# Performance work log

Hardware: AMD Instinct MI355X
Metric: run time of the kernel (lower is better)

The kernel has to match this reference:

```python
import jax, jax.numpy as jnp
import numpy as np

PAD0, PAD1 = 2, 1  # Blur pad=(2,1), replicate_pad=False -> upfirdn2d pad
UPSAMPLE_FACTOR = 2


def _make_kernel():
    k = jnp.array([1.0, 3.0, 3.0, 1.0], dtype=jnp.float32)
    k2 = k[None, :] * k[:, None]
    k2 = k2 / jnp.sum(k2)
    return k2 * (UPSAMPLE_FACTOR ** 2)  # (4,4)


def setup_inputs() -> dict:
    key = jax.random.key(0)
    x = jax.random.normal(key, (8, 256, 256, 256), dtype=jnp.float32)
    kernel = _make_kernel()
    return {"x": x, "kernel": kernel}


def reference(x, kernel):
    # upfirdn2d with up=1, down=1, pad=(PAD0, PAD1): zero-pad then true
    # convolution with the FIR kernel (flip == cross-correlation kernel).
    N, C, H, W = x.shape
    kh, kw = kernel.shape
    xp = jnp.pad(x, ((0, 0), (0, 0), (PAD0, PAD1), (PAD0, PAD1)))
    k = jnp.flip(kernel)[None, None, :, :]  # (1,1,kh,kw), true convolution
    # depthwise: fold channels into batch, single-channel conv
    xr = xp.reshape(N * C, 1, H + PAD0 + PAD1, W + PAD0 + PAD1)
    out = jax.lax.conv_general_dilated(
        xr, k, window_strides=(1, 1), padding='VALID',
        dimension_numbers=('NCHW', 'OIHW', 'NCHW'))
    Ho = H + PAD0 + PAD1 - kh + 1
    Wo = W + PAD0 + PAD1 - kw + 1
    return out.reshape(N, C, Ho, Wo)
```

## Files before the change

kernel.cpp:

```cpp
#include <hip/hip_runtime.h>


constexpr int W = 256;
constexpr int H = 256;
constexpr float F0 = 0.25f;
constexpr float F1 = 0.75f;

typedef float f32x4 __attribute__((ext_vector_type(4)));

__device__ __forceinline__ float4 hrow(const float* __restrict__ xp, int i,
                                       int lane, int col) {
    if ((unsigned)i >= (unsigned)H) return make_float4(0.f, 0.f, 0.f, 0.f);
    const float* r = xp + i * W;
    float4 v = *reinterpret_cast<const float4*>(r + col);
    float2 L = *reinterpret_cast<const float2*>(r + (lane ? col - 2 : 0));
    float  R = r[lane < 63 ? col + 4 : W - 1];
    if (lane == 0)  { L.x = 0.f; L.y = 0.f; }
    if (lane == 63) { R = 0.f; }
    float4 h;
    h.x = F0 * L.x + F1 * L.y + F1 * v.x + F0 * v.y;
    h.y = F0 * L.y + F1 * v.x + F1 * v.y + F0 * v.z;
    h.z = F0 * v.x + F1 * v.y + F1 * v.z + F0 * v.w;
    h.w = F0 * v.y + F1 * v.z + F1 * v.w + F0 * R;
    return h;
}

__global__ __launch_bounds__(256) void blur_kernel(const float* __restrict__ x,
                                                   float* __restrict__ out) {
    const int plane = blockIdx.x;
    const int wave  = threadIdx.x >> 6;
    const int lane  = threadIdx.x & 63;
    const float* xp = x + (size_t)plane * (H * W);
    float*       op = out + (size_t)plane * (H * W);
    const int r0  = wave * 64;
    const int col = lane * 4;

    float4 A = hrow(xp, r0 - 2, lane, col);
    float4 B = hrow(xp, r0 - 1, lane, col);
    float4 C = hrow(xp, r0,     lane, col);

#pragma unroll 8
    for (int t = 0; t < 64; ++t) {
        const int io = r0 + t;
        float4 D = hrow(xp, io + 1, lane, col);
        f32x4 o;
        o.x = F0 * (A.x + D.x) + F1 * (B.x + C.x);
        o.y = F0 * (A.y + D.y) + F1 * (B.y + C.y);
        o.z = F0 * (A.z + D.z) + F1 * (B.z + C.z);
        o.w = F0 * (A.w + D.w) + F1 * (B.w + C.w);
        __builtin_nontemporal_store(o, reinterpret_cast<f32x4*>(op + io * W + col));
        A = B; B = C; C = D;
    }
}

extern "C" void kernel_launch(void* const* d_in, const int* in_sizes, int n_in,
                              void* d_out, int out_size, void* d_ws, size_t ws_size,
                              hipStream_t stream) {
    const float* x = (const float*)d_in[0];
    float* o = (float*)d_out;
    const int planes = in_sizes[0] / (H * W);
    blur_kernel<<<planes, 256, 0, stream>>>(x, o);
}
```

Measured before the change: 235.4 us.

## Stream input rows into LDS via async global_load_lds with an 8-row ring buffer

Replaces the per-row direct global loads (a float4 plus halo float2 and scalar) with asynchronous global_load_lds transfers into a per-wave 8-row LDS ring. Explicit vmcnt waits keep several rows in flight, so load latency overlaps computation, and the halo values come from LDS instead of redundant global reads. Stores become regular rather than nontemporal. The hand-tuned vmcnt counts are fragile because stores also increment vmcnt, and the 32KB of LDS per block may limit occupancy.

```diff
diff --git a/kernel.cpp b/kernel.cpp
--- a/kernel.cpp
+++ b/kernel.cpp
@@ -8,25 +8,9 @@
 
 typedef float f32x4 __attribute__((ext_vector_type(4)));
 
-__device__ __forceinline__ float4 hrow(const float* __restrict__ xp, int i,
-                                       int lane, int col) {
-    if ((unsigned)i >= (unsigned)H) return make_float4(0.f, 0.f, 0.f, 0.f);
-    const float* r = xp + i * W;
-    float4 v = *reinterpret_cast<const float4*>(r + col);
-    float2 L = *reinterpret_cast<const float2*>(r + (lane ? col - 2 : 0));
-    float  R = r[lane < 63 ? col + 4 : W - 1];
-    if (lane == 0)  { L.x = 0.f; L.y = 0.f; }
-    if (lane == 63) { R = 0.f; }
-    float4 h;
-    h.x = F0 * L.x + F1 * L.y + F1 * v.x + F0 * v.y;
-    h.y = F0 * L.y + F1 * v.x + F1 * v.y + F0 * v.z;
-    h.z = F0 * v.x + F1 * v.y + F1 * v.z + F0 * v.w;
-    h.w = F0 * v.y + F1 * v.z + F1 * v.w + F0 * R;
-    return h;
-}
-
 __global__ __launch_bounds__(256) void blur_kernel(const float* __restrict__ x,
                                                    float* __restrict__ out) {
+    __shared__ float lds[4][8][W];
     const int plane = blockIdx.x;
     const int wave  = threadIdx.x >> 6;
     const int lane  = threadIdx.x & 63;
@@ -34,23 +18,72 @@
     float*       op = out + (size_t)plane * (H * W);
     const int r0  = wave * 64;
     const int col = lane * 4;
+    float* lbase = &lds[wave][0][0];
 
-    float4 A = hrow(xp, r0 - 2, lane, col);
-    float4 B = hrow(xp, r0 - 1, lane, col);
-    float4 C = hrow(xp, r0,     lane, col);
+    auto issue = [&](int row, int slot) {
+        const int rc = row < 0 ? 0 : (row > H - 1 ? H - 1 : row);
+        const float* g = xp + rc * W + col;
+        __builtin_amdgcn_global_load_lds(
+            (const __attribute__((address_space(1))) unsigned int*)g,
+            (__attribute__((address_space(3))) unsigned int*)(lbase + slot * W),
+            16, 0, 0);
+    };
 
-#pragma unroll 8
-    for (int t = 0; t < 64; ++t) {
-        const int io = r0 + t;
-        float4 D = hrow(xp, io + 1, lane, col);
-        f32x4 o;
-        o.x = F0 * (A.x + D.x) + F1 * (B.x + C.x);
-        o.y = F0 * (A.y + D.y) + F1 * (B.y + C.y);
-        o.z = F0 * (A.z + D.z) + F1 * (B.z + C.z);
-        o.w = F0 * (A.w + D.w) + F1 * (B.w + C.w);
-        __builtin_nontemporal_store(o, reinterpret_cast<f32x4*>(op + io * W + col));
-        A = B; B = C; C = D;
+    auto hrow = [&](int slot) -> float4 {
+        const float* rowp = lbase + slot * W;
+        float4 v = *reinterpret_cast<const float4*>(rowp + col);
+        float2 L = *reinterpret_cast<const float2*>(rowp + (lane ? col - 2 : 0));
+        float  R = rowp[lane < 63 ? col + 4 : 0];
+        if (lane == 0)  { L.x = 0.f; L.y = 0.f; }
+        if (lane == 63) { R = 0.f; }
+        float4 h;
+        h.x = F0 * L.x + F1 * L.y + F1 * v.x + F0 * v.y;
+        h.y = F0 * L.y + F1 * v.x + F1 * v.y + F0 * v.z;
+        h.z = F0 * v.x + F1 * v.y + F1 * v.z + F0 * v.w;
+        h.w = F0 * v.y + F1 * v.z + F1 * v.w + F0 * R;
+        return h;
+    };
+
+    #pragma unroll
+    for (int k = 0; k < 8; ++k) issue(r0 - 2 + k, k);
+
+    asm volatile("s_waitcnt vmcnt(5)" ::: "memory");
+    __builtin_amdgcn_sched_barrier(0);
+    float4 A = hrow(0);
+    float4 B = hrow(1);
+    float4 C = hrow(2);
+    if (r0 == 0) {
+        A.x = A.y = A.z = A.w = 0.f;
+        B.x = B.y = B.z = B.w = 0.f;
     }
+
+#define BLUR_ITER(T, WAITSTR)                                              \
+    {                                                                      \
+        const int io = r0 + (T);                                           \
+        asm volatile(WAITSTR ::: "memory");                                \
+        __builtin_amdgcn_sched_barrier(0);                                 \
+        float4 D = hrow(((T) + 3) & 7);                                    \
+        if (io + 1 >= H) { D.x = D.y = D.z = D.w = 0.f; }                  \
+        f32x4 o;                                                           \
+        o.x = F0 * (A.x + D.x) + F1 * (B.x + C.x);                         \
+        o.y = F0 * (A.y + D.y) + F1 * (B.y + C.y);                         \
+        o.z = F0 * (A.z + D.z) + F1 * (B.z + C.z);                         \
+        o.w = F0 * (A.w + D.w) + F1 * (B.w + C.w);                         \
+        issue(io + 6, (T) & 7);                                            \
+        *reinterpret_cast<f32x4*>(op + io * W + col) = o;                  \
+        A = B; B = C; C = D;                                               \
+    }
+
+    BLUR_ITER(0, "s_waitcnt vmcnt(4)");
+    BLUR_ITER(1, "s_waitcnt vmcnt(5)");
+    BLUR_ITER(2, "s_waitcnt vmcnt(6)");
+    BLUR_ITER(3, "s_waitcnt vmcnt(7)");
+    BLUR_ITER(4, "s_waitcnt vmcnt(8)");
+    #pragma unroll 4
+    for (int t = 5; t < 64; ++t) {
+        BLUR_ITER(t, "s_waitcnt vmcnt(9)");
+    }
+#undef BLUR_ITER
 }
 
 extern "C" void kernel_launch(void* const* d_in, const int* in_sizes, int n_in,
```

After: 231.9 us. No clear change (-1.5%).
